# Kernel tuning notes

Hardware: AMD Instinct MI355X
Metric: run time of the kernel (lower is better)

The kernel has to match this reference:

```python
import jax, jax.numpy as jnp
import numpy as np

B, S, D = 4, 2048, 1024  # batch, seq_len, d_model (d_in == d_model)


def setup_inputs() -> dict:
    key = jax.random.key(0)
    ks = jax.random.split(key, 9)
    scale = 1.0 / np.sqrt(D)
    return {
        "q": jax.random.normal(ks[0], (B, S, D), jnp.float32),
        "k": jax.random.normal(ks[1], (B, S, D), jnp.float32),
        "v": jax.random.normal(ks[2], (B, S, D), jnp.float32),
        "Wq": jax.random.normal(ks[3], (D, D), jnp.float32) * scale,
        "bq": jnp.zeros((D,), jnp.float32),
        "Wk": jax.random.normal(ks[4], (D, D), jnp.float32) * scale,
        "bk": jnp.zeros((D,), jnp.float32),
        "Wv": jax.random.normal(ks[5], (D, D), jnp.float32) * scale,
        "bv": jnp.zeros((D,), jnp.float32),
    }


def reference(q, k, v, Wq, bq, Wk, bk, Wv, bv):
    query = q @ Wq + bq                      # [B, S, D]
    key_p = k @ Wk + bk                      # [B, S, D]
    value = v @ Wv + bv                      # [B, S, D]
    inv_sqrt_d = 1.0 / jnp.sqrt(jnp.asarray(D, query.dtype))
    scores = jnp.einsum('bqd,bkd->bqk', query, key_p) * inv_sqrt_d  # [B, S, S]
    w = jax.nn.softmax(scores, axis=-1)
    return jnp.einsum('bqk,bkd->bqd', w, value)  # [B, S, D]
```

## Files before the change

### kernel.cpp

```cpp
#include <hip/hip_runtime.h>
#include <math.h>


using short8  = __attribute__((ext_vector_type(8))) short;
using floatx4 = __attribute__((ext_vector_type(4))) float;

__device__ __forceinline__ unsigned short f2bf(float f) {
    union { float f; unsigned u; } x; x.f = f;
    return (unsigned short)((x.u + 0x8000u) >> 16);
}

__device__ __forceinline__ void gload_lds16(const unsigned short* g, unsigned short* l) {
    __builtin_amdgcn_global_load_lds(
        (const __attribute__((address_space(1))) unsigned int*)g,
        (__attribute__((address_space(3))) unsigned int*)l, 16, 0, 0);
}

#define SBAR   __builtin_amdgcn_s_barrier()
#define LGKM0  asm volatile("s_waitcnt lgkmcnt(0)" ::: "memory")
#define VMW(n) asm volatile("s_waitcnt vmcnt(" #n ")" ::: "memory")

__global__ __launch_bounds__(256) void prep(
    const float* __restrict__ q, const float* __restrict__ k, const float* __restrict__ v,
    const float* __restrict__ W0, const float* __restrict__ W1, const float* __restrict__ W2,
    unsigned short* __restrict__ qkvbf, unsigned short* __restrict__ Wt)
{
    __shared__ float tile[32][33];
    const int id = blockIdx.x;
    const int t  = threadIdx.x;
    if (id < 24576) {
        const int z  = id >> 13;
        const int xb = id & 8191;
        const float* x = (z == 0) ? q : (z == 1) ? k : v;
        const size_t i = ((size_t)xb * 256 + t) * 4;
        const float4 a = *(const float4*)(x + i);
        ushort4 p = { f2bf(a.x), f2bf(a.y), f2bf(a.z), f2bf(a.w) };
        *(ushort4*)(qkvbf + (size_t)z * 8192 * 1024 + i) = p;
    } else {
        const int idt = id - 24576;
        const int z  = idt >> 10;
        const int r  = idt & 1023;
        const int bx = (r & 31) * 32;
        const int by = (r >> 5) * 32;
        const float* W = (z == 0) ? W0 : (z == 1) ? W1 : W2;
        unsigned short* o = Wt + (size_t)z * 1024 * 1024;
        const int tx = t & 31;
        const int ty = (t >> 5) * 4;
        #pragma unroll
        for (int rr = 0; rr < 4; ++rr)
            tile[ty + rr][tx] = W[(size_t)(by + ty + rr) * 1024 + bx + tx];
        __syncthreads();
        #pragma unroll
        for (int rr = 0; rr < 4; ++rr)
            o[(size_t)(bx + ty + rr) * 1024 + by + tx] = f2bf(tile[tx][ty + rr]);
    }
}


#define STAGE_A(bb, ks, tt) do { \
    const unsigned short* s_ = gA + (size_t)srow * lda + (tt) * 64 + (ks) * 32 + scol; \
    unsigned short* d_ = lds + (bb) * 32768 + (ks) * 8192 + t512 * 8; \
    gload_lds16(s_, d_); \
    gload_lds16(s_ + (size_t)128 * lda, d_ + 4096); \
} while (0)

#define STAGE_B(bb, ks, tt) do { \
    const unsigned short* s_ = gB + (size_t)srow * ldb + (tt) * 64 + (ks) * 32 + scol; \
    unsigned short* d_ = lds + (bb) * 32768 + 16384 + (ks) * 8192 + t512 * 8; \
    gload_lds16(s_, d_); \
    gload_lds16(s_ + (size_t)128 * ldb, d_ + 4096); \
} while (0)

#define LDSA(bb, ks, i) (*(const short8*)&lds[(bb) * 32768 + (ks) * 8192 + (arow + (i) * 16) * 32 + rslot])
#define LDSB(bb, ks, j) (*(const short8*)&lds[(bb) * 32768 + 16384 + (ks) * 8192 + (brow + (j) * 16) * 32 + rslot])

#define MFMA16(IB) do { \
    __builtin_amdgcn_s_setprio(1); \
    _Pragma("unroll") \
    for (int i_ = 0; i_ < 4; ++i_) \
        _Pragma("unroll") \
        for (int j_ = 0; j_ < 4; ++j_) \
            acc[(IB) + i_][j_] = __builtin_amdgcn_mfma_f32_16x16x32_bf16( \
                af[i_], bf[j_], acc[(IB) + i_][j_], 0, 0, 0); \
    __builtin_amdgcn_s_setprio(0); \
} while (0)

__device__ __forceinline__ void gemm8ph(
    const unsigned short* __restrict__ gA, int lda,
    const unsigned short* __restrict__ gB, int ldb,
    int nt, unsigned short* lds, floatx4 (&acc)[8][4])
{
    const int t512 = threadIdx.x;
    const int lane = t512 & 63;
    const int wave = t512 >> 6;
    const int wr   = wave >> 2;
    const int wc   = wave & 3;
    const int l15  = lane & 15;
    const int quad = lane >> 4;
    const int srow = t512 >> 2;
    const int scol = ((t512 & 3) ^ ((t512 >> 3) & 3)) * 8;
    const int rslot = (quad ^ ((l15 >> 1) & 3)) * 8;
    const int arow = wr * 128 + l15;
    const int brow = wc * 64 + l15;

    short8 af[4], bf[4];

    STAGE_B(0, 0, 0); STAGE_A(0, 0, 0); STAGE_B(0, 1, 0); STAGE_A(0, 1, 0);
    STAGE_B(1, 0, 1); STAGE_A(1, 0, 1); STAGE_B(1, 1, 1);
    VMW(10);
    SBAR;

    int b = 0;
    for (int t = 0; t < nt; ++t, b ^= 1) {
        #pragma unroll
        for (int j = 0; j < 4; ++j) bf[j] = LDSB(b, 0, j);
        #pragma unroll
        for (int i = 0; i < 4; ++i) af[i] = LDSA(b, 0, i);
        if (t + 1 < nt) STAGE_A(b ^ 1, 1, t + 1);
        SBAR; LGKM0;
        MFMA16(0);
        SBAR;
        #pragma unroll
        for (int i = 0; i < 4; ++i) af[i] = LDSA(b, 0, i + 4);
        if (t + 2 < nt) STAGE_B(b, 0, t + 2);
        SBAR; LGKM0;
        MFMA16(4);
        if (t == nt - 1)      VMW(0);
        else if (t == nt - 2) VMW(8);
        else                  VMW(10);
        SBAR;
        #pragma unroll
        for (int j = 0; j < 4; ++j) bf[j] = LDSB(b, 1, j);
        #pragma unroll
        for (int i = 0; i < 4; ++i) af[i] = LDSA(b, 1, i);
        if (t + 2 < nt) STAGE_A(b, 0, t + 2);
        SBAR; LGKM0;
        MFMA16(0);
        SBAR;
        #pragma unroll
        for (int i = 0; i < 4; ++i) af[i] = LDSA(b, 1, i + 4);
        if (t + 2 < nt) STAGE_B(b, 1, t + 2);
        SBAR; LGKM0;
        MFMA16(4);
        if (t + 1 < nt) {
            if (t + 1 == nt - 1) VMW(4);
            else                 VMW(10);
            SBAR;
        }
    }
}

#define EPI_IDS                                   \
    const int tt   = threadIdx.x;                 \
    const int lane = tt & 63;                     \
    const int wave = tt >> 6;                     \
    const int wr   = wave >> 2;                   \
    const int wc   = wave & 3;                    \
    const int l15  = lane & 15;                   \
    const int quad = lane >> 4;

__global__ __launch_bounds__(512, 2) void proj8(
    const unsigned short* __restrict__ Abf,
    const unsigned short* __restrict__ Wt,
    const float* __restrict__ bq, const float* __restrict__ bk, const float* __restrict__ bv,
    unsigned short* __restrict__ Qp, unsigned short* __restrict__ Kp,
    unsigned short* __restrict__ Vpt)
{
    __shared__ __attribute__((aligned(16))) unsigned short lds[65536];
    const int id = blockIdx.x;
    const int g  = (id & 7) * 48 + (id >> 3);
    const int z  = g >> 7;
    const int r  = g & 127;
    const int m0 = (r >> 2) * 256;
    const int n0 = (r & 3) * 256;

    const unsigned short* gA = Abf + (size_t)z * 8192 * 1024 + (size_t)m0 * 1024;
    const unsigned short* gB = Wt  + (size_t)z * 1024 * 1024 + (size_t)n0 * 1024;

    floatx4 acc[8][4] = {};
    gemm8ph(gA, 1024, gB, 1024, 16, lds, acc);

    EPI_IDS
    const float* bias = (z == 0) ? bq : (z == 1) ? bk : bv;
    #pragma unroll
    for (int j = 0; j < 4; ++j) {
        const int col = n0 + wc * 64 + j * 16 + l15;
        const float bv_ = bias[col];
        #pragma unroll
        for (int i = 0; i < 8; ++i) {
            const int row = m0 + wr * 128 + i * 16 + quad * 4;
            if (z < 2) {
                unsigned short* C = (z == 0) ? Qp : Kp;
                #pragma unroll
                for (int r2 = 0; r2 < 4; ++r2)
                    C[(size_t)(row + r2) * 1024 + col] = f2bf(acc[i][j][r2] + bv_);
            } else {
                ushort4 p = { f2bf(acc[i][j][0] + bv_), f2bf(acc[i][j][1] + bv_),
                              f2bf(acc[i][j][2] + bv_), f2bf(acc[i][j][3] + bv_) };
                *(ushort4*)&Vpt[(size_t)col * 8192 + row] = p;
            }
        }
    }
}

__global__ __launch_bounds__(512, 2) void scores8(
    const unsigned short* __restrict__ Qp,
    const unsigned short* __restrict__ Kp,
    unsigned short* __restrict__ Pexp,
    float* __restrict__ rowsum)
{
    __shared__ __attribute__((aligned(16))) unsigned short lds[65536];
    const int id = blockIdx.x;
    const int g  = (id & 7) * 32 + (id >> 3);
    const int z  = g >> 6;
    const int r  = g & 63;
    const int m0 = (r >> 3) * 256;
    const int n0 = (r & 7) * 256;

    const unsigned short* gA = Qp + (size_t)z * 2048 * 1024 + (size_t)m0 * 1024;
    const unsigned short* gB = Kp + (size_t)z * 2048 * 1024 + (size_t)n0 * 1024;

    floatx4 acc[8][4] = {};
    gemm8ph(gA, 1024, gB, 1024, 16, lds, acc);

    EPI_IDS
    unsigned short* P = Pexp + (size_t)z * 2048 * 2048;
    float* rs = rowsum + (size_t)z * 2048;
    #pragma unroll
    for (int i = 0; i < 8; ++i) {
        const int rowb = m0 + wr * 128 + i * 16 + quad * 4;
        float sm[4] = {0.f, 0.f, 0.f, 0.f};
        #pragma unroll
        for (int j = 0; j < 4; ++j) {
            const int col = n0 + wc * 64 + j * 16 + l15;
            #pragma unroll
            for (int r2 = 0; r2 < 4; ++r2) {
                const float p = __expf(acc[i][j][r2] * 0.03125f);
                sm[r2] += p;
                P[(size_t)(rowb + r2) * 2048 + col] = f2bf(p);
            }
        }
        #pragma unroll
        for (int r2 = 0; r2 < 4; ++r2) {
            float s = sm[r2];
            s += __shfl_xor(s, 1);
            s += __shfl_xor(s, 2);
            s += __shfl_xor(s, 4);
            s += __shfl_xor(s, 8);
            if (l15 == 0)
                atomicAdd(&rs[rowb + r2], s);
        }
    }
}

__global__ __launch_bounds__(512, 2) void pv8(
    const unsigned short* __restrict__ Pexp,
    const unsigned short* __restrict__ Vpt,
    const float* __restrict__ rowsum,
    float* __restrict__ out)
{
    __shared__ __attribute__((aligned(16))) unsigned short lds[65536];
    const int id = blockIdx.x;
    const int g  = (id & 7) * 16 + (id >> 3);
    const int z  = g >> 5;
    const int r  = g & 31;
    const int m0 = (r >> 2) * 256;
    const int n0 = (r & 3) * 256;

    const unsigned short* gA = Pexp + (size_t)z * 2048 * 2048 + (size_t)m0 * 2048;
    const unsigned short* gB = Vpt  + (size_t)n0 * 8192 + (size_t)z * 2048;

    floatx4 acc[8][4] = {};
    gemm8ph(gA, 2048, gB, 8192, 32, lds, acc);

    EPI_IDS
    const float* rs = rowsum + (size_t)z * 2048;
    float* C = out + (size_t)z * 2048 * 1024;
    #pragma unroll
    for (int i = 0; i < 8; ++i) {
        const int rowb = m0 + wr * 128 + i * 16 + quad * 4;
        float inv[4];
        #pragma unroll
        for (int r2 = 0; r2 < 4; ++r2) inv[r2] = 1.0f / rs[rowb + r2];
        #pragma unroll
        for (int j = 0; j < 4; ++j) {
            const int col = n0 + wc * 64 + j * 16 + l15;
            #pragma unroll
            for (int r2 = 0; r2 < 4; ++r2)
                C[(size_t)(rowb + r2) * 1024 + col] = acc[i][j][r2] * inv[r2];
        }
    }
}

extern "C" void kernel_launch(void* const* d_in, const int* in_sizes, int n_in,
                              void* d_out, int out_size, void* d_ws, size_t ws_size,
                              hipStream_t stream)
{
    const float* q  = (const float*)d_in[0];
    const float* k  = (const float*)d_in[1];
    const float* v  = (const float*)d_in[2];
    const float* Wq = (const float*)d_in[3];
    const float* bq = (const float*)d_in[4];
    const float* Wk = (const float*)d_in[5];
    const float* bk = (const float*)d_in[6];
    const float* Wv = (const float*)d_in[7];
    const float* bv = (const float*)d_in[8];
    float* out = (float*)d_out;

    const int Bn = 4, S = 2048;

    char* w = (char*)d_ws;
    unsigned short* Wt     = (unsigned short*)(w);
    unsigned short* Qp     = (unsigned short*)(w + (6u << 20));
    unsigned short* Kp     = (unsigned short*)(w + (22u << 20));
    unsigned short* Vpt    = (unsigned short*)(w + (38u << 20));
    unsigned short* qkvbf  = (unsigned short*)(w + (54u << 20));
    unsigned short* Pexp   = (unsigned short*)(w + (54u << 20));
    float*          rowsum = (float*)(w + (86u << 20));

    hipMemsetAsync(rowsum, 0, (size_t)Bn * S * sizeof(float), stream);

    prep<<<dim3(27648), dim3(256), 0, stream>>>(q, k, v, Wq, Wk, Wv, qkvbf, Wt);

    proj8<<<dim3(384), dim3(512), 0, stream>>>(qkvbf, Wt, bq, bk, bv, Qp, Kp, Vpt);

    scores8<<<dim3(256), dim3(512), 0, stream>>>(Qp, Kp, Pexp, rowsum);

    pv8<<<dim3(128), dim3(512), 0, stream>>>(Pexp, Vpt, rowsum, out);
}
```

Baseline: 331.8 us.

## Halve GEMM M-tile to 128x256 and double grid sizes for better CU fill

The shared GEMM core changes from 256x256 tiles to 128x256 tiles, with a simpler two-phase pipeline that stages A and B halves together. LDS per block shrinks from 128KB to 96KB, the accumulator shrinks to 4x4, and every launch grid doubles, so the PV kernel (previously 128 blocks on a 256-CU part) can occupy more CUs. The cost is lower arithmetic intensity per block, meaning more global and L2 traffic for B tiles, plus a rewritten wait-count and barrier schedule. The occupancy hint in launch bounds is also removed.

```diff
diff --git a/kernel.cpp b/kernel.cpp
--- a/kernel.cpp
+++ b/kernel.cpp
@@ -57,38 +57,36 @@
 }
 
 
-#define STAGE_A(bb, ks, tt) do { \
-    const unsigned short* s_ = gA + (size_t)srow * lda + (tt) * 64 + (ks) * 32 + scol; \
-    unsigned short* d_ = lds + (bb) * 32768 + (ks) * 8192 + t512 * 8; \
-    gload_lds16(s_, d_); \
-    gload_lds16(s_ + (size_t)128 * lda, d_ + 4096); \
+#define STAGE_A(bb, kh, tt) do { \
+    gload_lds16(gA + (size_t)srowA * lda + (tt) * 64 + (kh) * 32 + scol, \
+                lds + (bb) * 24576 + (kh) * 4096 + t512 * 8); \
 } while (0)
 
-#define STAGE_B(bb, ks, tt) do { \
-    const unsigned short* s_ = gB + (size_t)srow * ldb + (tt) * 64 + (ks) * 32 + scol; \
-    unsigned short* d_ = lds + (bb) * 32768 + 16384 + (ks) * 8192 + t512 * 8; \
+#define STAGE_B(bb, kh, tt) do { \
+    const unsigned short* s_ = gB + (size_t)srowA * ldb + (tt) * 64 + (kh) * 32 + scol; \
+    unsigned short* d_ = lds + (bb) * 24576 + 8192 + (kh) * 8192 + t512 * 8; \
     gload_lds16(s_, d_); \
     gload_lds16(s_ + (size_t)128 * ldb, d_ + 4096); \
 } while (0)
 
-#define LDSA(bb, ks, i) (*(const short8*)&lds[(bb) * 32768 + (ks) * 8192 + (arow + (i) * 16) * 32 + rslot])
-#define LDSB(bb, ks, j) (*(const short8*)&lds[(bb) * 32768 + 16384 + (ks) * 8192 + (brow + (j) * 16) * 32 + rslot])
-
-#define MFMA16(IB) do { \
+#define LDSA(bb, kh, i) (*(const short8*)&lds[(bb) * 24576 + (kh) * 4096 + (arow + (i) * 16) * 32 + rslot])
+#define LDSB(bb, kh, j) (*(const short8*)&lds[(bb) * 24576 + 8192 + (kh) * 8192 + (brow + (j) * 16) * 32 + rslot])
+
+#define MFMA16 do { \
     __builtin_amdgcn_s_setprio(1); \
     _Pragma("unroll") \
     for (int i_ = 0; i_ < 4; ++i_) \
         _Pragma("unroll") \
         for (int j_ = 0; j_ < 4; ++j_) \
-            acc[(IB) + i_][j_] = __builtin_amdgcn_mfma_f32_16x16x32_bf16( \
-                af[i_], bf[j_], acc[(IB) + i_][j_], 0, 0, 0); \
+            acc[i_][j_] = __builtin_amdgcn_mfma_f32_16x16x32_bf16( \
+                af[i_], bf[j_], acc[i_][j_], 0, 0, 0); \
     __builtin_amdgcn_s_setprio(0); \
 } while (0)
 
-__device__ __forceinline__ void gemm8ph(
+__device__ __forceinline__ void gemm2ph(
     const unsigned short* __restrict__ gA, int lda,
     const unsigned short* __restrict__ gB, int ldb,
-    int nt, unsigned short* lds, floatx4 (&acc)[8][4])
+    int nt, unsigned short* lds, floatx4 (&acc)[4][4])
 {
     const int t512 = threadIdx.x;
     const int lane = t512 & 63;
@@ -97,17 +95,18 @@
     const int wc   = wave & 3;
     const int l15  = lane & 15;
     const int quad = lane >> 4;
-    const int srow = t512 >> 2;
-    const int scol = ((t512 & 3) ^ ((t512 >> 3) & 3)) * 8;
+    const int srowA = t512 >> 2;
+    const int scol  = ((t512 & 3) ^ ((t512 >> 3) & 3)) * 8;
     const int rslot = (quad ^ ((l15 >> 1) & 3)) * 8;
-    const int arow = wr * 128 + l15;
-    const int brow = wc * 64 + l15;
+    const int arow  = wr * 64 + l15;
+    const int brow  = wc * 64 + l15;
 
     short8 af[4], bf[4];
 
-    STAGE_B(0, 0, 0); STAGE_A(0, 0, 0); STAGE_B(0, 1, 0); STAGE_A(0, 1, 0);
-    STAGE_B(1, 0, 1); STAGE_A(1, 0, 1); STAGE_B(1, 1, 1);
-    VMW(10);
+    STAGE_A(0, 0, 0); STAGE_B(0, 0, 0);
+    STAGE_A(0, 1, 0); STAGE_B(0, 1, 0);
+    STAGE_A(1, 0, 1); STAGE_B(1, 0, 1);
+    VMW(6);
     SBAR;
 
     int b = 0;
@@ -116,35 +115,20 @@
         for (int j = 0; j < 4; ++j) bf[j] = LDSB(b, 0, j);
         #pragma unroll
         for (int i = 0; i < 4; ++i) af[i] = LDSA(b, 0, i);
-        if (t + 1 < nt) STAGE_A(b ^ 1, 1, t + 1);
+        if (t + 1 < nt) { STAGE_A(b ^ 1, 1, t + 1); STAGE_B(b ^ 1, 1, t + 1); }
         SBAR; LGKM0;
-        MFMA16(0);
+        MFMA16;
+        if (t < nt - 1) VMW(6); else VMW(0);
         SBAR;
         #pragma unroll
-        for (int i = 0; i < 4; ++i) af[i] = LDSA(b, 0, i + 4);
-        if (t + 2 < nt) STAGE_B(b, 0, t + 2);
+        for (int j = 0; j < 4; ++j) bf[j] = LDSB(b, 1, j);
+        #pragma unroll
+        for (int i = 0; i < 4; ++i) af[i] = LDSA(b, 1, i);
+        if (t + 2 < nt) { STAGE_A(b, 0, t + 2); STAGE_B(b, 0, t + 2); }
         SBAR; LGKM0;
-        MFMA16(4);
-        if (t == nt - 1)      VMW(0);
-        else if (t == nt - 2) VMW(8);
-        else                  VMW(10);
-        SBAR;
-        #pragma unroll
-        for (int j = 0; j < 4; ++j) bf[j] = LDSB(b, 1, j);
-        #pragma unroll
-        for (int i = 0; i < 4; ++i) af[i] = LDSA(b, 1, i);
-        if (t + 2 < nt) STAGE_A(b, 0, t + 2);
-        SBAR; LGKM0;
-        MFMA16(0);
-        SBAR;
-        #pragma unroll
-        for (int i = 0; i < 4; ++i) af[i] = LDSA(b, 1, i + 4);
-        if (t + 2 < nt) STAGE_B(b, 1, t + 2);
-        SBAR; LGKM0;
-        MFMA16(4);
-        if (t + 1 < nt) {
-            if (t + 1 == nt - 1) VMW(4);
-            else                 VMW(10);
+        MFMA16;
+        if (t < nt - 1) {
+            if (t + 2 < nt) VMW(6); else VMW(3);
             SBAR;
         }
     }
@@ -159,26 +143,26 @@
     const int l15  = lane & 15;                   \
     const int quad = lane >> 4;
 
-__global__ __launch_bounds__(512, 2) void proj8(
+__global__ __launch_bounds__(512) void proj8(
     const unsigned short* __restrict__ Abf,
     const unsigned short* __restrict__ Wt,
     const float* __restrict__ bq, const float* __restrict__ bk, const float* __restrict__ bv,
     unsigned short* __restrict__ Qp, unsigned short* __restrict__ Kp,
     unsigned short* __restrict__ Vpt)
 {
-    __shared__ __attribute__((aligned(16))) unsigned short lds[65536];
+    __shared__ __attribute__((aligned(16))) unsigned short lds[49152];
     const int id = blockIdx.x;
-    const int g  = (id & 7) * 48 + (id >> 3);
-    const int z  = g >> 7;
-    const int r  = g & 127;
-    const int m0 = (r >> 2) * 256;
+    const int g  = (id & 7) * 96 + (id >> 3);
+    const int z  = g >> 8;
+    const int r  = g & 255;
+    const int m0 = (r >> 2) * 128;
     const int n0 = (r & 3) * 256;
 
     const unsigned short* gA = Abf + (size_t)z * 8192 * 1024 + (size_t)m0 * 1024;
     const unsigned short* gB = Wt  + (size_t)z * 1024 * 1024 + (size_t)n0 * 1024;
 
-    floatx4 acc[8][4] = {};
-    gemm8ph(gA, 1024, gB, 1024, 16, lds, acc);
+    floatx4 acc[4][4] = {};
+    gemm2ph(gA, 1024, gB, 1024, 16, lds, acc);
 
     EPI_IDS
     const float* bias = (z == 0) ? bq : (z == 1) ? bk : bv;
@@ -187,8 +171,8 @@
         const int col = n0 + wc * 64 + j * 16 + l15;
         const float bv_ = bias[col];
         #pragma unroll
-        for (int i = 0; i < 8; ++i) {
-            const int row = m0 + wr * 128 + i * 16 + quad * 4;
+        for (int i = 0; i < 4; ++i) {
+            const int row = m0 + wr * 64 + i * 16 + quad * 4;
             if (z < 2) {
                 unsigned short* C = (z == 0) ? Qp : Kp;
                 #pragma unroll
@@ -203,32 +187,32 @@
     }
 }
 
-__global__ __launch_bounds__(512, 2) void scores8(
+__global__ __launch_bounds__(512) void scores8(
     const unsigned short* __restrict__ Qp,
     const unsigned short* __restrict__ Kp,
     unsigned short* __restrict__ Pexp,
     float* __restrict__ rowsum)
 {
-    __shared__ __attribute__((aligned(16))) unsigned short lds[65536];
+    __shared__ __attribute__((aligned(16))) unsigned short lds[49152];
     const int id = blockIdx.x;
-    const int g  = (id & 7) * 32 + (id >> 3);
-    const int z  = g >> 6;
-    const int r  = g & 63;
-    const int m0 = (r >> 3) * 256;
+    const int g  = (id & 7) * 64 + (id >> 3);
+    const int z  = g >> 7;
+    const int r  = g & 127;
+    const int m0 = (r >> 3) * 128;
     const int n0 = (r & 7) * 256;
 
     const unsigned short* gA = Qp + (size_t)z * 2048 * 1024 + (size_t)m0 * 1024;
     const unsigned short* gB = Kp + (size_t)z * 2048 * 1024 + (size_t)n0 * 1024;
 
-    floatx4 acc[8][4] = {};
-    gemm8ph(gA, 1024, gB, 1024, 16, lds, acc);
+    floatx4 acc[4][4] = {};
+    gemm2ph(gA, 1024, gB, 1024, 16, lds, acc);
 
     EPI_IDS
     unsigned short* P = Pexp + (size_t)z * 2048 * 2048;
     float* rs = rowsum + (size_t)z * 2048;
     #pragma unroll
-    for (int i = 0; i < 8; ++i) {
-        const int rowb = m0 + wr * 128 + i * 16 + quad * 4;
+    for (int i = 0; i < 4; ++i) {
+        const int rowb = m0 + wr * 64 + i * 16 + quad * 4;
         float sm[4] = {0.f, 0.f, 0.f, 0.f};
         #pragma unroll
         for (int j = 0; j < 4; ++j) {
@@ -253,32 +237,32 @@
     }
 }
 
-__global__ __launch_bounds__(512, 2) void pv8(
+__global__ __launch_bounds__(512) void pv8(
     const unsigned short* __restrict__ Pexp,
     const unsigned short* __restrict__ Vpt,
     const float* __restrict__ rowsum,
     float* __restrict__ out)
 {
-    __shared__ __attribute__((aligned(16))) unsigned short lds[65536];
+    __shared__ __attribute__((aligned(16))) unsigned short lds[49152];
     const int id = blockIdx.x;
-    const int g  = (id & 7) * 16 + (id >> 3);
-    const int z  = g >> 5;
-    const int r  = g & 31;
-    const int m0 = (r >> 2) * 256;
+    const int g  = (id & 7) * 32 + (id >> 3);
+    const int z  = g >> 6;
+    const int r  = g & 63;
+    const int m0 = (r >> 2) * 128;
     const int n0 = (r & 3) * 256;
 
     const unsigned short* gA = Pexp + (size_t)z * 2048 * 2048 + (size_t)m0 * 2048;
     const unsigned short* gB = Vpt  + (size_t)n0 * 8192 + (size_t)z * 2048;
 
-    floatx4 acc[8][4] = {};
-    gemm8ph(gA, 2048, gB, 8192, 32, lds, acc);
+    floatx4 acc[4][4] = {};
+    gemm2ph(gA, 2048, gB, 8192, 32, lds, acc);
 
     EPI_IDS
     const float* rs = rowsum + (size_t)z * 2048;
     float* C = out + (size_t)z * 2048 * 1024;
     #pragma unroll
-    for (int i = 0; i < 8; ++i) {
-        const int rowb = m0 + wr * 128 + i * 16 + quad * 4;
+    for (int i = 0; i < 4; ++i) {
+        const int rowb = m0 + wr * 64 + i * 16 + quad * 4;
         float inv[4];
         #pragma unroll
         for (int r2 = 0; r2 < 4; ++r2) inv[r2] = 1.0f / rs[rowb + r2];
@@ -322,9 +306,9 @@
 
     prep<<<dim3(27648), dim3(256), 0, stream>>>(q, k, v, Wq, Wk, Wv, qkvbf, Wt);
 
-    proj8<<<dim3(384), dim3(512), 0, stream>>>(qkvbf, Wt, bq, bk, bv, Qp, Kp, Vpt);
-
-    scores8<<<dim3(256), dim3(512), 0, stream>>>(Qp, Kp, Pexp, rowsum);
-
-    pv8<<<dim3(128), dim3(512), 0, stream>>>(Pexp, Vpt, rowsum, out);
-}
+    proj8<<<dim3(768), dim3(512), 0, stream>>>(qkvbf, Wt, bq, bk, bv, Qp, Kp, Vpt);
+
+    scores8<<<dim3(512), dim3(512), 0, stream>>>(Qp, Kp, Pexp, rowsum);
+
+    pv8<<<dim3(256), dim3(512), 0, stream>>>(Pexp, Vpt, rowsum, out);
+}
```

Measured after the change: 310.2 us. -6.5%, faster.

## Stage GEMM epilogues through LDS for vectorized stores and re-pipeline K loop

Applied to the files above, without the earlier changes.

All three GEMM epilogues (projection, scores/exp, PV) now write accumulator tiles into a padded LDS buffer in 32-row slabs, then emit coalesced 8- or 16-byte global stores instead of scattered 2-byte/4-byte per-lane writes. The main K loop is restructured to prefetch the whole next K tile into the alternate buffer with simpler vmcnt waits and sched_barriers around MFMA blocks. The occupancy hint of 2 blocks per CU is dropped from launch bounds. This adds extra barriers and LDS traffic in the epilogue and may change register allocation.

```diff
diff --git a/kernel.cpp b/kernel.cpp
--- a/kernel.cpp
+++ b/kernel.cpp
@@ -16,9 +16,12 @@
         (__attribute__((address_space(3))) unsigned int*)l, 16, 0, 0);
 }
 
-#define SBAR   __builtin_amdgcn_s_barrier()
-#define LGKM0  asm volatile("s_waitcnt lgkmcnt(0)" ::: "memory")
-#define VMW(n) asm volatile("s_waitcnt vmcnt(" #n ")" ::: "memory")
+#define SBAR    __builtin_amdgcn_s_barrier()
+#define SCHEDB  __builtin_amdgcn_sched_barrier(0)
+#define PRIO1   __builtin_amdgcn_s_setprio(1)
+#define PRIO0   __builtin_amdgcn_s_setprio(0)
+#define LGKM(n) asm volatile("s_waitcnt lgkmcnt(" #n ")" ::: "memory")
+#define VMW(n)  asm volatile("s_waitcnt vmcnt(" #n ")" ::: "memory")
 
 __global__ __launch_bounds__(256) void prep(
     const float* __restrict__ q, const float* __restrict__ k, const float* __restrict__ v,
@@ -57,35 +60,35 @@
 }
 
 
-#define STAGE_A(bb, ks, tt) do { \
-    const unsigned short* s_ = gA + (size_t)srow * lda + (tt) * 64 + (ks) * 32 + scol; \
-    unsigned short* d_ = lds + (bb) * 32768 + (ks) * 8192 + t512 * 8; \
+#define STAGE_A(bb, kh, tt) do { \
+    const unsigned short* s_ = gA + (size_t)srowA * lda + (tt) * 64 + (kh) * 32 + scol; \
+    unsigned short* d_ = lds + (bb) * 32768 + (kh) * 8192 + t512 * 8; \
     gload_lds16(s_, d_); \
     gload_lds16(s_ + (size_t)128 * lda, d_ + 4096); \
 } while (0)
 
-#define STAGE_B(bb, ks, tt) do { \
-    const unsigned short* s_ = gB + (size_t)srow * ldb + (tt) * 64 + (ks) * 32 + scol; \
-    unsigned short* d_ = lds + (bb) * 32768 + 16384 + (ks) * 8192 + t512 * 8; \
+#define STAGE_B(bb, kh, tt) do { \
+    const unsigned short* s_ = gB + (size_t)srowA * ldb + (tt) * 64 + (kh) * 32 + scol; \
+    unsigned short* d_ = lds + (bb) * 32768 + 16384 + (kh) * 8192 + t512 * 8; \
     gload_lds16(s_, d_); \
     gload_lds16(s_ + (size_t)128 * ldb, d_ + 4096); \
 } while (0)
 
-#define LDSA(bb, ks, i) (*(const short8*)&lds[(bb) * 32768 + (ks) * 8192 + (arow + (i) * 16) * 32 + rslot])
-#define LDSB(bb, ks, j) (*(const short8*)&lds[(bb) * 32768 + 16384 + (ks) * 8192 + (brow + (j) * 16) * 32 + rslot])
-
-#define MFMA16(IB) do { \
-    __builtin_amdgcn_s_setprio(1); \
+#define LDSA(bb, kh, i) (*(const short8*)&lds[(bb) * 32768 + (kh) * 8192 + (arow + (i) * 16) * 32 + rslot])
+#define LDSB(bb, kh, j) (*(const short8*)&lds[(bb) * 32768 + 16384 + (kh) * 8192 + (brow + (j) * 16) * 32 + rslot])
+
+#define MM4x4(IB) do { \
+    PRIO1; \
     _Pragma("unroll") \
     for (int i_ = 0; i_ < 4; ++i_) \
         _Pragma("unroll") \
         for (int j_ = 0; j_ < 4; ++j_) \
             acc[(IB) + i_][j_] = __builtin_amdgcn_mfma_f32_16x16x32_bf16( \
                 af[i_], bf[j_], acc[(IB) + i_][j_], 0, 0, 0); \
-    __builtin_amdgcn_s_setprio(0); \
+    PRIO0; \
 } while (0)
 
-__device__ __forceinline__ void gemm8ph(
+__device__ __forceinline__ void gemm256(
     const unsigned short* __restrict__ gA, int lda,
     const unsigned short* __restrict__ gB, int ldb,
     int nt, unsigned short* lds, floatx4 (&acc)[8][4])
@@ -97,56 +100,52 @@
     const int wc   = wave & 3;
     const int l15  = lane & 15;
     const int quad = lane >> 4;
-    const int srow = t512 >> 2;
-    const int scol = ((t512 & 3) ^ ((t512 >> 3) & 3)) * 8;
+    const int srowA = t512 >> 2;
+    const int scol  = ((t512 & 3) ^ ((t512 >> 3) & 3)) * 8;
     const int rslot = (quad ^ ((l15 >> 1) & 3)) * 8;
-    const int arow = wr * 128 + l15;
-    const int brow = wc * 64 + l15;
+    const int arow  = wr * 128 + l15;
+    const int brow  = wc * 64 + l15;
 
     short8 af[4], bf[4];
 
-    STAGE_B(0, 0, 0); STAGE_A(0, 0, 0); STAGE_B(0, 1, 0); STAGE_A(0, 1, 0);
-    STAGE_B(1, 0, 1); STAGE_A(1, 0, 1); STAGE_B(1, 1, 1);
-    VMW(10);
+    STAGE_A(0, 0, 0); STAGE_B(0, 0, 0);
+    STAGE_A(0, 1, 0); STAGE_B(0, 1, 0);
+    STAGE_A(1, 0, 1); STAGE_B(1, 0, 1);
+    VMW(8);
     SBAR;
 
-    int b = 0;
-    for (int t = 0; t < nt; ++t, b ^= 1) {
-        #pragma unroll
-        for (int j = 0; j < 4; ++j) bf[j] = LDSB(b, 0, j);
-        #pragma unroll
-        for (int i = 0; i < 4; ++i) af[i] = LDSA(b, 0, i);
-        if (t + 1 < nt) STAGE_A(b ^ 1, 1, t + 1);
-        SBAR; LGKM0;
-        MFMA16(0);
-        SBAR;
-        #pragma unroll
-        for (int i = 0; i < 4; ++i) af[i] = LDSA(b, 0, i + 4);
-        if (t + 2 < nt) STAGE_B(b, 0, t + 2);
-        SBAR; LGKM0;
-        MFMA16(4);
-        if (t == nt - 1)      VMW(0);
-        else if (t == nt - 2) VMW(8);
-        else                  VMW(10);
-        SBAR;
-        #pragma unroll
-        for (int j = 0; j < 4; ++j) bf[j] = LDSB(b, 1, j);
-        #pragma unroll
-        for (int i = 0; i < 4; ++i) af[i] = LDSA(b, 1, i);
-        if (t + 2 < nt) STAGE_A(b, 0, t + 2);
-        SBAR; LGKM0;
-        MFMA16(0);
-        SBAR;
-        #pragma unroll
-        for (int i = 0; i < 4; ++i) af[i] = LDSA(b, 1, i + 4);
-        if (t + 2 < nt) STAGE_B(b, 1, t + 2);
-        SBAR; LGKM0;
-        MFMA16(4);
-        if (t + 1 < nt) {
-            if (t + 1 == nt - 1) VMW(4);
-            else                 VMW(10);
-            SBAR;
-        }
+    int p = 0;
+    for (int t = 0; t < nt; ++t, p ^= 1) {
+        #pragma unroll
+        for (int j = 0; j < 4; ++j) bf[j] = LDSB(p, 0, j);
+        #pragma unroll
+        for (int i = 0; i < 4; ++i) af[i] = LDSA(p, 0, i);
+        if (t >= 1 && t + 1 < nt) STAGE_A(p ^ 1, 0, t + 1);
+        SBAR; LGKM(0); SCHEDB;
+        MM4x4(0);
+        SBAR;
+        #pragma unroll
+        for (int i = 0; i < 4; ++i) af[i] = LDSA(p, 0, i + 4);
+        if (t >= 1 && t + 1 < nt) STAGE_B(p ^ 1, 0, t + 1);
+        SBAR; LGKM(0); SCHEDB;
+        MM4x4(4);
+        if (t + 1 < nt) { VMW(4); } else { VMW(0); }
+        SBAR;
+        #pragma unroll
+        for (int j = 0; j < 4; ++j) bf[j] = LDSB(p, 1, j);
+        #pragma unroll
+        for (int i = 0; i < 4; ++i) af[i] = LDSA(p, 1, i);
+        if (t + 1 < nt) STAGE_A(p ^ 1, 1, t + 1);
+        SBAR; LGKM(0); SCHEDB;
+        MM4x4(0);
+        SBAR;
+        #pragma unroll
+        for (int i = 0; i < 4; ++i) af[i] = LDSA(p, 1, i + 4);
+        if (t + 1 < nt) STAGE_B(p ^ 1, 1, t + 1);
+        SBAR; LGKM(0); SCHEDB;
+        MM4x4(4);
+        if (t + 1 < nt) { VMW(4); }
+        SBAR;
     }
 }
 
@@ -159,7 +158,7 @@
     const int l15  = lane & 15;                   \
     const int quad = lane >> 4;
 
-__global__ __launch_bounds__(512, 2) void proj8(
+__global__ __launch_bounds__(512) void proj8(
     const unsigned short* __restrict__ Abf,
     const unsigned short* __restrict__ Wt,
     const float* __restrict__ bq, const float* __restrict__ bk, const float* __restrict__ bv,
@@ -178,32 +177,50 @@
     const unsigned short* gB = Wt  + (size_t)z * 1024 * 1024 + (size_t)n0 * 1024;
 
     floatx4 acc[8][4] = {};
-    gemm8ph(gA, 1024, gB, 1024, 16, lds, acc);
+    gemm256(gA, 1024, gB, 1024, 16, lds, acc);
 
     EPI_IDS
     const float* bias = (z == 0) ? bq : (z == 1) ? bk : bv;
+    float bvj[4];
     #pragma unroll
-    for (int j = 0; j < 4; ++j) {
-        const int col = n0 + wc * 64 + j * 16 + l15;
-        const float bv_ = bias[col];
-        #pragma unroll
-        for (int i = 0; i < 8; ++i) {
-            const int row = m0 + wr * 128 + i * 16 + quad * 4;
-            if (z < 2) {
-                unsigned short* C = (z == 0) ? Qp : Kp;
+    for (int j = 0; j < 4; ++j) bvj[j] = bias[n0 + wc * 64 + j * 16 + l15];
+
+    unsigned short (*sst)[264] = (unsigned short (*)[264])lds;
+    for (int s = 0; s < 8; ++s) {
+        if (wr == (s >> 2)) {
+            const int i0 = (s & 3) * 2;
+            #pragma unroll
+            for (int ii = 0; ii < 2; ++ii)
                 #pragma unroll
-                for (int r2 = 0; r2 < 4; ++r2)
-                    C[(size_t)(row + r2) * 1024 + col] = f2bf(acc[i][j][r2] + bv_);
-            } else {
-                ushort4 p = { f2bf(acc[i][j][0] + bv_), f2bf(acc[i][j][1] + bv_),
-                              f2bf(acc[i][j][2] + bv_), f2bf(acc[i][j][3] + bv_) };
-                *(ushort4*)&Vpt[(size_t)col * 8192 + row] = p;
+                for (int j = 0; j < 4; ++j)
+                    #pragma unroll
+                    for (int r2 = 0; r2 < 4; ++r2)
+                        sst[ii * 16 + quad * 4 + r2][wc * 64 + j * 16 + l15] =
+                            f2bf(acc[i0 + ii][j][r2] + bvj[j]);
+        }
+        SBAR;
+        if (z < 2) {
+            unsigned short* C = (z == 0) ? Qp : Kp;
+            #pragma unroll
+            for (int c = 0; c < 4; ++c) {
+                const int a = c * 512 + tt, lr = a >> 6, cc = a & 63;
+                *(ushort4*)(C + (size_t)(m0 + s * 32 + lr) * 1024 + n0 + cc * 4) =
+                    *(const ushort4*)&sst[lr][cc * 4];
             }
-        }
-    }
-}
-
-__global__ __launch_bounds__(512, 2) void scores8(
+        } else {
+            #pragma unroll
+            for (int c = 0; c < 4; ++c) {
+                const int a = c * 512 + tt, col = a >> 3, ch = a & 7;
+                ushort4 pk = { sst[ch * 4 + 0][col], sst[ch * 4 + 1][col],
+                               sst[ch * 4 + 2][col], sst[ch * 4 + 3][col] };
+                *(ushort4*)(Vpt + (size_t)(n0 + col) * 8192 + m0 + s * 32 + ch * 4) = pk;
+            }
+        }
+        SBAR;
+    }
+}
+
+__global__ __launch_bounds__(512) void scores8(
     const unsigned short* __restrict__ Qp,
     const unsigned short* __restrict__ Kp,
     unsigned short* __restrict__ Pexp,
@@ -221,39 +238,61 @@
     const unsigned short* gB = Kp + (size_t)z * 2048 * 1024 + (size_t)n0 * 1024;
 
     floatx4 acc[8][4] = {};
-    gemm8ph(gA, 1024, gB, 1024, 16, lds, acc);
+    gemm256(gA, 1024, gB, 1024, 16, lds, acc);
 
     EPI_IDS
     unsigned short* P = Pexp + (size_t)z * 2048 * 2048;
     float* rs = rowsum + (size_t)z * 2048;
+
     #pragma unroll
     for (int i = 0; i < 8; ++i) {
         const int rowb = m0 + wr * 128 + i * 16 + quad * 4;
         float sm[4] = {0.f, 0.f, 0.f, 0.f};
         #pragma unroll
-        for (int j = 0; j < 4; ++j) {
-            const int col = n0 + wc * 64 + j * 16 + l15;
+        for (int j = 0; j < 4; ++j)
             #pragma unroll
             for (int r2 = 0; r2 < 4; ++r2) {
-                const float p = __expf(acc[i][j][r2] * 0.03125f);
-                sm[r2] += p;
-                P[(size_t)(rowb + r2) * 2048 + col] = f2bf(p);
+                const float pv_ = __expf(acc[i][j][r2] * 0.03125f);
+                acc[i][j][r2] = pv_;
+                sm[r2] += pv_;
             }
-        }
         #pragma unroll
         for (int r2 = 0; r2 < 4; ++r2) {
-            float s = sm[r2];
-            s += __shfl_xor(s, 1);
-            s += __shfl_xor(s, 2);
-            s += __shfl_xor(s, 4);
-            s += __shfl_xor(s, 8);
+            float sv = sm[r2];
+            sv += __shfl_xor(sv, 1);
+            sv += __shfl_xor(sv, 2);
+            sv += __shfl_xor(sv, 4);
+            sv += __shfl_xor(sv, 8);
             if (l15 == 0)
-                atomicAdd(&rs[rowb + r2], s);
-        }
-    }
-}
-
-__global__ __launch_bounds__(512, 2) void pv8(
+                atomicAdd(&rs[rowb + r2], sv);
+        }
+    }
+
+    unsigned short (*sst)[264] = (unsigned short (*)[264])lds;
+    for (int s = 0; s < 8; ++s) {
+        if (wr == (s >> 2)) {
+            const int i0 = (s & 3) * 2;
+            #pragma unroll
+            for (int ii = 0; ii < 2; ++ii)
+                #pragma unroll
+                for (int j = 0; j < 4; ++j)
+                    #pragma unroll
+                    for (int r2 = 0; r2 < 4; ++r2)
+                        sst[ii * 16 + quad * 4 + r2][wc * 64 + j * 16 + l15] =
+                            f2bf(acc[i0 + ii][j][r2]);
+        }
+        SBAR;
+        #pragma unroll
+        for (int c = 0; c < 4; ++c) {
+            const int a = c * 512 + tt, lr = a >> 6, cc = a & 63;
+            *(ushort4*)(P + (size_t)(m0 + s * 32 + lr) * 2048 + n0 + cc * 4) =
+                *(const ushort4*)&sst[lr][cc * 4];
+        }
+        SBAR;
+    }
+}
+
+__global__ __launch_bounds__(512) void pv8(
     const unsigned short* __restrict__ Pexp,
     const unsigned short* __restrict__ Vpt,
     const float* __restrict__ rowsum,
@@ -271,24 +310,38 @@
     const unsigned short* gB = Vpt  + (size_t)n0 * 8192 + (size_t)z * 2048;
 
     floatx4 acc[8][4] = {};
-    gemm8ph(gA, 2048, gB, 8192, 32, lds, acc);
+    gemm256(gA, 2048, gB, 8192, 32, lds, acc);
 
     EPI_IDS
     const float* rs = rowsum + (size_t)z * 2048;
     float* C = out + (size_t)z * 2048 * 1024;
-    #pragma unroll
-    for (int i = 0; i < 8; ++i) {
-        const int rowb = m0 + wr * 128 + i * 16 + quad * 4;
-        float inv[4];
-        #pragma unroll
-        for (int r2 = 0; r2 < 4; ++r2) inv[r2] = 1.0f / rs[rowb + r2];
-        #pragma unroll
-        for (int j = 0; j < 4; ++j) {
-            const int col = n0 + wc * 64 + j * 16 + l15;
-            #pragma unroll
-            for (int r2 = 0; r2 < 4; ++r2)
-                C[(size_t)(rowb + r2) * 1024 + col] = acc[i][j][r2] * inv[r2];
-        }
+
+    float (*sstF)[264] = (float (*)[264])lds;
+    for (int s = 0; s < 8; ++s) {
+        if (wr == (s >> 2)) {
+            const int i0 = (s & 3) * 2;
+            #pragma unroll
+            for (int ii = 0; ii < 2; ++ii) {
+                const int rowb = m0 + wr * 128 + (i0 + ii) * 16 + quad * 4;
+                float inv[4];
+                #pragma unroll
+                for (int r2 = 0; r2 < 4; ++r2) inv[r2] = 1.0f / rs[rowb + r2];
+                #pragma unroll
+                for (int j = 0; j < 4; ++j)
+                    #pragma unroll
+                    for (int r2 = 0; r2 < 4; ++r2)
+                        sstF[ii * 16 + quad * 4 + r2][wc * 64 + j * 16 + l15] =
+                            acc[i0 + ii][j][r2] * inv[r2];
+            }
+        }
+        SBAR;
+        #pragma unroll
+        for (int c = 0; c < 4; ++c) {
+            const int a = c * 512 + tt, lr = a >> 6, cc = a & 63;
+            *(float4*)(C + (size_t)(m0 + s * 32 + lr) * 1024 + n0 + cc * 4) =
+                *(const float4*)&sstF[lr][cc * 4];
+        }
+        SBAR;
     }
 }
 
```

Measured after the change: 328.0 us. No clear change (-1.2%).
